# Kernel tuning notes

Measured on AMD Instinct MI355X. Metric: run time of the kernel, lower is better.

Reference implementation:

```python
import jax, jax.numpy as jnp
import numpy as np
from jax.scipy.special import gammaln

REG = 1e-6
NHLOG2PI = -0.5 * float(np.log(2.0 * np.pi))


def _log_besseli(s, kappa):
    # Uniform asymptotic expansion (leading order) of log I_s(kappa):
    # I_s(s*x) ~ exp(s*eta) / (sqrt(2*pi*s) * (1+x^2)^(1/4))
    x = kappa / s
    sq = jnp.sqrt(1.0 + x * x)
    eta = sq + jnp.log(x) - jnp.log1p(sq)
    return s * eta - 0.5 * jnp.log(2.0 * jnp.pi * s) - 0.5 * jnp.log(sq)


def _log_C_vmf(d, kappa):
    # log C_d(kappa) = d*(-0.5 log 2pi) + s*log(kappa) - log I_s(kappa), s = d/2 - 1
    s = 0.5 * d - 1.0
    return d * NHLOG2PI + s * jnp.log(kappa) - _log_besseli(s, kappa)


def _log_surface_area(dim):
    # HypersphericalUniform.__log_surface_area
    h = (dim + 1.0) / 2.0
    return np.log(2.0) + h * np.log(np.pi) - float(jax.scipy.special.gammaln(jnp.asarray(h, jnp.float32)))


def _vmf_layer(x, w_mu, w_logk, b_mu, b_logk, in_f, out_f):
    # eval mode: weight = mu (unit-normalized flat vector), reshape(in,out).T
    mu_w = w_mu / jnp.linalg.norm(w_mu)
    mu_b = b_mu / jnp.linalg.norm(b_mu)
    W = mu_w.reshape(in_f, out_f).T  # [out, in]
    y = x @ W.T + mu_b
    kw = jnp.exp(w_logk) + REG
    kb = jnp.exp(b_logk) + REG
    d_w = float(out_f * in_f)
    d_b = float(out_f)
    # log q(w) = kappa * <mu, w> + log C_d(kappa); here w = mu so <mu,w> = 1 (computed faithfully)
    lvp = (kw * jnp.dot(mu_w, mu_w) + _log_C_vmf(d_w, kw)
           + kb * jnp.dot(mu_b, mu_b) + _log_C_vmf(d_b, kb))
    # NOTE: source bug preserved -- bias prior also uses dim = out*in
    lp = -_log_surface_area(d_w) - _log_surface_area(d_w)
    return y, lvp, lp


def _gaussian_last_layer(x, w_mu, w_rho, b_mu, b_rho):
    # eval mode: weight = mu, bias = mu
    y = x @ w_mu.T + b_mu
    sw = jnp.log1p(jnp.exp(w_rho))
    sb = jnp.log1p(jnp.exp(b_rho))
    # log q at mu: (-log sqrt(2pi) - log sigma - 0).sum()
    lvp = jnp.sum(NHLOG2PI - jnp.log(sw)) + jnp.sum(NHLOG2PI - jnp.log(sb))
    # prior: PI=1, sigma1=1 -> standard normal logpdf summed
    lp = jnp.sum(NHLOG2PI - 0.5 * w_mu ** 2) + jnp.sum(NHLOG2PI - 0.5 * b_mu ** 2)
    return y, lvp, lp


def setup_inputs() -> dict:
    key = jax.random.key(0)
    ks = jax.random.split(key, 13)
    B, IN, H, OUT = 1024, 4096, 4096, 5
    return {
        "x": jax.random.normal(ks[0], (B, IN), jnp.float32),
        "w1_mu": jax.random.normal(ks[1], (H * IN,), jnp.float32),
        "w1_logkappa": jnp.float32(2.0),
        "b1_mu": jax.random.normal(ks[2], (H,), jnp.float32),
        "b1_logkappa": jnp.float32(2.0),
        "w2_mu": jax.random.normal(ks[3], (H * H,), jnp.float32),
        "w2_logkappa": jnp.float32(2.0),
        "b2_mu": jax.random.normal(ks[4], (H,), jnp.float32),
        "b2_logkappa": jnp.float32(2.0),
        "w3_mu": jax.random.uniform(ks[5], (OUT, H), jnp.float32, -0.2, 0.2),
        "w3_rho": jax.random.uniform(ks[6], (OUT, H), jnp.float32, -5.0, -4.0),
        "b3_mu": jax.random.uniform(ks[7], (OUT,), jnp.float32, -0.2, 0.2),
        "b3_rho": jax.random.uniform(ks[8], (OUT,), jnp.float32, -5.0, -4.0),
    }


def reference(x, w1_mu, w1_logkappa, b1_mu, b1_logkappa,
              w2_mu, w2_logkappa, b2_mu, b2_logkappa,
              w3_mu, w3_rho, b3_mu, b3_rho):
    IN, H, OUT = 4096, 4096, 5
    h1, lvp1, lp1 = _vmf_layer(x, w1_mu, w1_logkappa, b1_mu, b1_logkappa, IN, H)
    h1 = jax.nn.relu(h1)
    h2, lvp2, lp2 = _vmf_layer(h1, w2_mu, w2_logkappa, b2_mu, b2_logkappa, H, H)
    h2 = jax.nn.relu(h2)
    y, lvp3, lp3 = _gaussian_last_layer(h2, w3_mu, w3_rho, b3_mu, b3_rho)
    out = jax.nn.log_softmax(y, axis=-1)
    log_var_post = lvp1 + lvp2 + lvp3
    log_prior = lp1 + lp2 + lp3
    return out, log_var_post, jnp.asarray(log_prior, out.dtype)
```

## Files before the change

kernel.cpp:

```cpp
#include <hip/hip_runtime.h>
#include <cstdint>


#define NH (-0.9189385332046727)
#define DPI 3.141592653589793238462643383279502884

typedef short s16x8 __attribute__((ext_vector_type(8)));
typedef float f32x4 __attribute__((ext_vector_type(4)));

static __device__ __forceinline__ ushort f2bf(float f) {
  uint32_t u = __float_as_uint(f);
  u += 0x7fffu + ((u >> 16) & 1u);
  return (ushort)(u >> 16);
}
static __device__ __forceinline__ float bf2f(ushort h) {
  return __uint_as_float(((uint32_t)h) << 16);
}

static __device__ __forceinline__ void gload16(const void* g, void* l) {
  __builtin_amdgcn_global_load_lds(
      (__attribute__((address_space(1))) void*)g,
      (__attribute__((address_space(3))) void*)l,
      16, 0, 0);
}

__global__ void reduce_k(const float* __restrict__ x, int n,
                         double* __restrict__ part, int mode) {
  double a = 0.0;
  const int tid = blockIdx.x * blockDim.x + threadIdx.x;
  const int stride = gridDim.x * blockDim.x;
  const int n4 = n >> 2;
  for (int i = tid; i < n4; i += stride) {
    float4 v = reinterpret_cast<const float4*>(x)[i];
    if (mode == 0) {
      a += (double)v.x * v.x + (double)v.y * v.y +
           (double)v.z * v.z + (double)v.w * v.w;
    } else {
      a += log(log1p(exp((double)v.x)));
      a += log(log1p(exp((double)v.y)));
      a += log(log1p(exp((double)v.z)));
      a += log(log1p(exp((double)v.w)));
    }
  }
  for (int i = (n4 << 2) + tid; i < n; i += stride) {
    float v = x[i];
    a += (mode == 0) ? (double)v * v : log(log1p(exp((double)v)));
  }
  for (int o = 32; o > 0; o >>= 1) a += __shfl_down(a, o);
  __shared__ double red[4];
  if ((threadIdx.x & 63) == 0) red[threadIdx.x >> 6] = a;
  __syncthreads();
  if (threadIdx.x == 0) part[blockIdx.x] = red[0] + red[1] + red[2] + red[3];
}

__global__ void norms_k(const double* __restrict__ pw, int nw,
                        const double* __restrict__ pb, int nb,
                        float* __restrict__ out2) {
  __shared__ double red[4];
  const int t = threadIdx.x;
  double s[2];
  const double* p[2] = {pw, pb};
  const int   cn[2] = {nw, nb};
  for (int q = 0; q < 2; q++) {
    double v = 0.0;
    for (int i = t; i < cn[q]; i += 256) v += p[q][i];
    for (int o = 32; o > 0; o >>= 1) v += __shfl_down(v, o);
    if ((t & 63) == 0) red[t >> 6] = v;
    __syncthreads();
    s[q] = red[0] + red[1] + red[2] + red[3];
    __syncthreads();
  }
  if (t == 0) {
    out2[0] = (float)(1.0 / sqrt(s[0]));
    out2[1] = (float)(1.0 / sqrt(s[1]));
  }
}

static __device__ double logC_vmf(double d, double kappa) {
  double s  = 0.5 * d - 1.0;
  double x  = kappa / s;
  double sq = sqrt(1.0 + x * x);
  double eta = sq + log(x) - log1p(sq);
  double lb  = s * eta - 0.5 * log(2.0 * DPI * s) - 0.5 * log(sq);
  return d * NH + s * log(kappa) - lb;
}

__global__ void finalize_k(const double* __restrict__ P,
                           const float* lkw1, const float* lkb1,
                           const float* lkw2, const float* lkb2,
                           float* __restrict__ out_sc) {
  __shared__ double S[8];
  __shared__ double red[4];
  const int offs[8] = {0, 16384, 8192, 16392, 16400, 16408, 16409, 16417};
  const int cnts[8] = {8192, 8, 8192, 8, 8, 1, 8, 1};
  const int t = threadIdx.x;
  for (int ai = 0; ai < 8; ai++) {
    double v = 0.0;
    for (int i = t; i < cnts[ai]; i += 256) v += P[offs[ai] + i];
    for (int o = 32; o > 0; o >>= 1) v += __shfl_down(v, o);
    if ((t & 63) == 0) red[t >> 6] = v;
    __syncthreads();
    if (t == 0) S[ai] = red[0] + red[1] + red[2] + red[3];
    __syncthreads();
  }
  if (t == 0) {
    double Sw3 = S[4], Sb3 = S[5], R6 = S[6], R7 = S[7];
    const double dw = 16777216.0, db = 4096.0;
    double kw1 = exp((double)lkw1[0]) + 1e-6;
    double kb1 = exp((double)lkb1[0]) + 1e-6;
    double kw2 = exp((double)lkw2[0]) + 1e-6;
    double kb2 = exp((double)lkb2[0]) + 1e-6;
    double lvp = kw1 + logC_vmf(dw, kw1) + kb1 + logC_vmf(db, kb1)
               + kw2 + logC_vmf(dw, kw2) + kb2 + logC_vmf(db, kb2)
               + 20485.0 * NH - R6 - R7;
    double h64 = (dw + 1.0) * 0.5;
    double hf  = (double)(float)h64;
    double lsa = log(2.0) + h64 * log(DPI) - lgamma(hf);
    double lp  = -4.0 * lsa + 20485.0 * NH - 0.5 * (Sw3 + Sb3);
    out_sc[0] = (float)lvp;
    out_sc[1] = (float)lp;
  }
}

__global__ void split_plain_k(const float* __restrict__ in,
                              ushort* __restrict__ hi, ushort* __restrict__ lo,
                              int n4) {
  int i = blockIdx.x * blockDim.x + threadIdx.x;
  if (i >= n4) return;
  float4 v = reinterpret_cast<const float4*>(in)[i];
  ushort4 h, l;
  h.x = f2bf(v.x); l.x = f2bf(v.x - bf2f(h.x));
  h.y = f2bf(v.y); l.y = f2bf(v.y - bf2f(h.y));
  h.z = f2bf(v.z); l.z = f2bf(v.z - bf2f(h.z));
  h.w = f2bf(v.w); l.w = f2bf(v.w - bf2f(h.w));
  reinterpret_cast<ushort4*>(hi)[i] = h;
  reinterpret_cast<ushort4*>(lo)[i] = l;
}

__global__ void split_transpose_k(const float* __restrict__ in,
                                  ushort* __restrict__ hi,
                                  ushort* __restrict__ lo,
                                  double* __restrict__ part) {
  __shared__ float tile[64][33];
  __shared__ double red[4];
  const int tx = threadIdx.x, ty = threadIdx.y;
  const int n0 = blockIdx.x * 32, k0 = blockIdx.y * 64;
  double a = 0.0;
#pragma unroll
  for (int r = 0; r < 8; r++) {
    float v = in[(size_t)(k0 + ty + r * 8) * 4096 + n0 + tx];
    tile[ty + r * 8][tx] = v;
    a += (double)v * v;
  }
  __syncthreads();
#pragma unroll
  for (int r = 0; r < 4; r++) {
    const int nn = ty + r * 8;
    float v0 = tile[2 * tx][nn];
    float v1 = tile[2 * tx + 1][nn];
    ushort2 h, l;
    h.x = f2bf(v0); l.x = f2bf(v0 - bf2f(h.x));
    h.y = f2bf(v1); l.y = f2bf(v1 - bf2f(h.y));
    size_t o = ((size_t)(n0 + nn) * 4096 + k0 + 2 * tx) >> 1;
    reinterpret_cast<ushort2*>(hi)[o] = h;
    reinterpret_cast<ushort2*>(lo)[o] = l;
  }
  const int tid = ty * 32 + tx;
  for (int o = 32; o > 0; o >>= 1) a += __shfl_down(a, o);
  if ((tid & 63) == 0) red[tid >> 6] = a;
  __syncthreads();
  if (tid == 0)
    part[blockIdx.y * gridDim.x + blockIdx.x] = red[0] + red[1] + red[2] + red[3];
}

__global__ __launch_bounds__(256) void gemm_split_k(
    const ushort* __restrict__ Ahi, const ushort* __restrict__ Alo,
    const ushort* __restrict__ Bhi, const ushort* __restrict__ Blo,
    const float* __restrict__ bias, const float* __restrict__ scales,
    ushort* __restrict__ Ohi, ushort* __restrict__ Olo,
    float* __restrict__ Of,
    int M, int N, int K, int mode) {
  __shared__ ushort As[2][2][64 * 32];
  __shared__ ushort Bs[2][2][128 * 32];
  const int t = threadIdx.x;
  const int lane = t & 63, wid = t >> 6;
  const int wm = wid >> 1, wn = wid & 1;
  const int bm = blockIdx.y, bn = blockIdx.x;
  const int lr = lane & 15, lk = (lane >> 4) * 8;

  f32x4 acc[2][4];
#pragma unroll
  for (int i = 0; i < 2; i++)
#pragma unroll
    for (int j = 0; j < 4; j++) acc[i][j] = (f32x4){0.f, 0.f, 0.f, 0.f};

  const size_t arow = (size_t)(bm * 64) * K;
  const size_t brow = (size_t)(bn * 128) * K;
  const int ar = t >> 2, ac = (t & 3) * 8;

  auto STAGE = [&](int buf, int k0) {
    const size_t ga = arow + (size_t)ar * K + k0 + ac;
    gload16(Ahi + ga, &As[buf][0][t * 8]);
    gload16(Alo + ga, &As[buf][1][t * 8]);
#pragma unroll
    for (int q = 0; q < 2; q++) {
      const int L = q * 256 + t;
      const size_t gb = brow + (size_t)(L >> 2) * K + k0 + (L & 3) * 8;
      gload16(Bhi + gb, &Bs[buf][0][L * 8]);
      gload16(Blo + gb, &Bs[buf][1][L * 8]);
    }
  };

  auto COMPUTE = [&](int buf) {
    s16x8 ah[2], al[2], bh[4], bl[4];
#pragma unroll
    for (int i = 0; i < 2; i++) {
      const int ra = (wm * 32 + i * 16 + lr) * 32 + lk;
      ah[i] = *(const s16x8*)&As[buf][0][ra];
      al[i] = *(const s16x8*)&As[buf][1][ra];
    }
#pragma unroll
    for (int j = 0; j < 4; j++) {
      const int rb = (wn * 64 + j * 16 + lr) * 32 + lk;
      bh[j] = *(const s16x8*)&Bs[buf][0][rb];
      bl[j] = *(const s16x8*)&Bs[buf][1][rb];
    }
#pragma unroll
    for (int i = 0; i < 2; i++)
#pragma unroll
      for (int j = 0; j < 4; j++) {
        acc[i][j] = __builtin_amdgcn_mfma_f32_16x16x32_bf16(ah[i], bh[j], acc[i][j], 0, 0, 0);
        acc[i][j] = __builtin_amdgcn_mfma_f32_16x16x32_bf16(ah[i], bl[j], acc[i][j], 0, 0, 0);
        acc[i][j] = __builtin_amdgcn_mfma_f32_16x16x32_bf16(al[i], bh[j], acc[i][j], 0, 0, 0);
      }
  };

  STAGE(0, 0);
  __syncthreads();
  int cur = 0;
  for (int k0 = 32; k0 < K; k0 += 32) {
    STAGE(cur ^ 1, k0);
    COMPUTE(cur);
    __syncthreads();
    cur ^= 1;
  }
  COMPUTE(cur);

  const float wsc = scales[0], bsc = scales[1];
  const int rb0 = bm * 64 + wm * 32 + (lane >> 4) * 4;
  const int cb0 = bn * 128 + wn * 64 + lr;
#pragma unroll
  for (int j = 0; j < 4; j++) {
    const int col = cb0 + j * 16;
    const float bv = bias[col] * bsc;
#pragma unroll
    for (int i = 0; i < 2; i++) {
#pragma unroll
      for (int r = 0; r < 4; r++) {
        const int row = rb0 + i * 16 + r;
        float v = fmaxf(fmaf(acc[i][j][r], wsc, bv), 0.0f);
        const size_t o = (size_t)row * N + col;
        if (mode == 0) {
          ushort h = f2bf(v);
          Ohi[o] = h;
          Olo[o] = f2bf(v - bf2f(h));
        } else {
          Of[o] = v;
        }
      }
    }
  }
}

__global__ void layer3_k(const float* __restrict__ h2,
                         const float* __restrict__ w3,
                         const float* __restrict__ b3,
                         float* __restrict__ out) {
  const int row = blockIdx.x;
  const int t = threadIdx.x;
  const float* hr = h2 + (size_t)row * 4096;
  float a[5] = {0.f, 0.f, 0.f, 0.f, 0.f};
  for (int k = t; k < 4096; k += 256) {
    const float h = hr[k];
#pragma unroll
    for (int o = 0; o < 5; o++) a[o] += h * w3[o * 4096 + k];
  }
#pragma unroll
  for (int o = 0; o < 5; o++)
    for (int s = 32; s > 0; s >>= 1) a[o] += __shfl_down(a[o], s);
  __shared__ float red[4][5];
  if ((t & 63) == 0) {
#pragma unroll
    for (int o = 0; o < 5; o++) red[t >> 6][o] = a[o];
  }
  __syncthreads();
  if (t == 0) {
    float y[5];
#pragma unroll
    for (int o = 0; o < 5; o++)
      y[o] = red[0][o] + red[1][o] + red[2][o] + red[3][o] + b3[o];
    float m = y[0];
    for (int o = 1; o < 5; o++) m = fmaxf(m, y[o]);
    float ssum = 0.f;
    for (int o = 0; o < 5; o++) ssum += expf(y[o] - m);
    const float ls = m + logf(ssum);
    for (int o = 0; o < 5; o++) out[row * 5 + o] = y[o] - ls;
  }
}

extern "C" void kernel_launch(void* const* d_in, const int* in_sizes, int n_in,
                              void* d_out, int out_size, void* d_ws, size_t ws_size,
                              hipStream_t stream) {
  const float* x     = (const float*)d_in[0];
  const float* w1mu  = (const float*)d_in[1];
  const float* lkw1  = (const float*)d_in[2];
  const float* b1mu  = (const float*)d_in[3];
  const float* lkb1  = (const float*)d_in[4];
  const float* w2mu  = (const float*)d_in[5];
  const float* lkw2  = (const float*)d_in[6];
  const float* b2mu  = (const float*)d_in[7];
  const float* lkb2  = (const float*)d_in[8];
  const float* w3mu  = (const float*)d_in[9];
  const float* w3rho = (const float*)d_in[10];
  const float* b3mu  = (const float*)d_in[11];
  const float* b3rho = (const float*)d_in[12];
  float* outp = (float*)d_out;

  char* w = (char*)d_ws;
  double* P    = (double*)w;
  double* Pw1  = P;
  double* Pw2  = P + 8192;
  double* Pb1  = P + 16384;
  double* Pb2  = P + 16392;
  double* Pw3  = P + 16400;
  double* Pb3  = P + 16408;
  double* Pr3  = P + 16409;
  double* Pbr3 = P + 16417;
  float* params = (float*)(w + 140 * 1024);
  ushort* xhi  = (ushort*)(w + 256 * 1024);
  ushort* xlo  = xhi  + (size_t)1024 * 4096;
  ushort* h1hi = xlo  + (size_t)1024 * 4096;
  ushort* h1lo = h1hi + (size_t)1024 * 4096;
  ushort* wthi = (ushort*)(h1lo + (size_t)1024 * 4096);
  ushort* wtlo = wthi + (size_t)4096 * 4096;
  float*  h2   = (float*)xhi;

  split_plain_k<<<4096, 256, 0, stream>>>(x, xhi, xlo, 1048576);
  split_transpose_k<<<dim3(128, 64), dim3(32, 8), 0, stream>>>(w1mu, wthi, wtlo, Pw1);
  reduce_k<<<8, 256, 0, stream>>>(b1mu, 4096, Pb1, 0);
  reduce_k<<<8, 256, 0, stream>>>(w3mu, 20480, Pw3, 0);
  reduce_k<<<1, 256, 0, stream>>>(b3mu, 5, Pb3, 0);
  reduce_k<<<8, 256, 0, stream>>>(w3rho, 20480, Pr3, 1);
  reduce_k<<<1, 256, 0, stream>>>(b3rho, 5, Pbr3, 1);
  norms_k<<<1, 256, 0, stream>>>(Pw1, 8192, Pb1, 8, params + 0);
  gemm_split_k<<<dim3(32, 16), 256, 0, stream>>>(xhi, xlo, wthi, wtlo,
                                                 b1mu, params + 0,
                                                 h1hi, h1lo, nullptr,
                                                 1024, 4096, 4096, 0);
  split_transpose_k<<<dim3(128, 64), dim3(32, 8), 0, stream>>>(w2mu, wthi, wtlo, Pw2);
  reduce_k<<<8, 256, 0, stream>>>(b2mu, 4096, Pb2, 0);
  norms_k<<<1, 256, 0, stream>>>(Pw2, 8192, Pb2, 8, params + 2);
  gemm_split_k<<<dim3(32, 16), 256, 0, stream>>>(h1hi, h1lo, wthi, wtlo,
                                                 b2mu, params + 2,
                                                 nullptr, nullptr, h2,
                                                 1024, 4096, 4096, 1);
  finalize_k<<<1, 256, 0, stream>>>(P, lkw1, lkb1, lkw2, lkb2, outp + 5120);
  layer3_k<<<1024, 256, 0, stream>>>(h2, w3mu, b3mu, outp);
}
```

Measured before the change: 568.4 us.

## Split GEMM K dimension in two with combine kernel and merge small reductions

Adds a split-K mode to the bf16x3 GEMM, launching twice as many blocks that each cover half of K. The blocks write fp32 partials, and a separate combine kernel applies scale, bias, ReLU and the hi/lo split. The goal is better CU occupancy for a 512-block grid. LDS double buffering is removed in favour of a single-buffer loop with two barriers. Small reductions are merged into one launch. The change adds partial-buffer traffic and loses the load/compute overlap, and it is gated on workspace size.

```diff
diff --git a/kernel.cpp b/kernel.cpp
--- a/kernel.cpp
+++ b/kernel.cpp
@@ -24,25 +24,24 @@
       16, 0, 0);
 }
 
-__global__ void reduce_k(const float* __restrict__ x, int n,
-                         double* __restrict__ part, int mode) {
+__global__ void small_reduce_k(const float* __restrict__ b1,
+                               const float* __restrict__ b2,
+                               const float* __restrict__ w3,
+                               const float* __restrict__ b3,
+                               const float* __restrict__ r3,
+                               const float* __restrict__ br3,
+                               double* __restrict__ P) {
+  const int bid = blockIdx.x;
+  const float* x; int n, lb, nb, mode; double* out;
+  if (bid < 8)        { x = b1;  n = 4096;  lb = bid;      nb = 8; mode = 0; out = P + 16384; }
+  else if (bid < 16)  { x = b2;  n = 4096;  lb = bid - 8;  nb = 8; mode = 0; out = P + 16392; }
+  else if (bid < 24)  { x = w3;  n = 20480; lb = bid - 16; nb = 8; mode = 0; out = P + 16400; }
+  else if (bid == 24) { x = b3;  n = 5;     lb = 0;        nb = 1; mode = 0; out = P + 16408; }
+  else if (bid < 33)  { x = r3;  n = 20480; lb = bid - 25; nb = 8; mode = 1; out = P + 16409; }
+  else                { x = br3; n = 5;     lb = 0;        nb = 1; mode = 1; out = P + 16417; }
   double a = 0.0;
-  const int tid = blockIdx.x * blockDim.x + threadIdx.x;
-  const int stride = gridDim.x * blockDim.x;
-  const int n4 = n >> 2;
-  for (int i = tid; i < n4; i += stride) {
-    float4 v = reinterpret_cast<const float4*>(x)[i];
-    if (mode == 0) {
-      a += (double)v.x * v.x + (double)v.y * v.y +
-           (double)v.z * v.z + (double)v.w * v.w;
-    } else {
-      a += log(log1p(exp((double)v.x)));
-      a += log(log1p(exp((double)v.y)));
-      a += log(log1p(exp((double)v.z)));
-      a += log(log1p(exp((double)v.w)));
-    }
-  }
-  for (int i = (n4 << 2) + tid; i < n; i += stride) {
+  const int tid = lb * 256 + threadIdx.x, stride = nb * 256;
+  for (int i = tid; i < n; i += stride) {
     float v = x[i];
     a += (mode == 0) ? (double)v * v : log(log1p(exp((double)v)));
   }
@@ -50,7 +49,7 @@
   __shared__ double red[4];
   if ((threadIdx.x & 63) == 0) red[threadIdx.x >> 6] = a;
   __syncthreads();
-  if (threadIdx.x == 0) part[blockIdx.x] = red[0] + red[1] + red[2] + red[3];
+  if (threadIdx.x == 0) out[lb] = red[0] + red[1] + red[2] + red[3];
 }
 
 __global__ void norms_k(const double* __restrict__ pw, int nw,
@@ -179,9 +178,9 @@
     const float* __restrict__ bias, const float* __restrict__ scales,
     ushort* __restrict__ Ohi, ushort* __restrict__ Olo,
     float* __restrict__ Of,
-    int M, int N, int K, int mode) {
-  __shared__ ushort As[2][2][64 * 32];
-  __shared__ ushort Bs[2][2][128 * 32];
+    int M, int N, int K, int ksize, int mode) {
+  __shared__ ushort As[2][64 * 32];
+  __shared__ ushort Bs[2][128 * 32];
   const int t = threadIdx.x;
   const int lane = t & 63, wid = t >> 6;
   const int wm = wid >> 1, wn = wid & 1;
@@ -197,33 +196,35 @@
   const size_t arow = (size_t)(bm * 64) * K;
   const size_t brow = (size_t)(bn * 128) * K;
   const int ar = t >> 2, ac = (t & 3) * 8;
-
-  auto STAGE = [&](int buf, int k0) {
-    const size_t ga = arow + (size_t)ar * K + k0 + ac;
-    gload16(Ahi + ga, &As[buf][0][t * 8]);
-    gload16(Alo + ga, &As[buf][1][t * 8]);
+  const int kbeg = blockIdx.z * ksize;
+  const int kend = kbeg + ksize;
+
+  for (int k0 = kbeg; k0 < kend; k0 += 32) {
+    {
+      const size_t ga = arow + (size_t)ar * K + k0 + ac;
+      gload16(Ahi + ga, &As[0][t * 8]);
+      gload16(Alo + ga, &As[1][t * 8]);
+    }
 #pragma unroll
     for (int q = 0; q < 2; q++) {
       const int L = q * 256 + t;
       const size_t gb = brow + (size_t)(L >> 2) * K + k0 + (L & 3) * 8;
-      gload16(Bhi + gb, &Bs[buf][0][L * 8]);
-      gload16(Blo + gb, &Bs[buf][1][L * 8]);
-    }
-  };
-
-  auto COMPUTE = [&](int buf) {
+      gload16(Bhi + gb, &Bs[0][L * 8]);
+      gload16(Blo + gb, &Bs[1][L * 8]);
+    }
+    __syncthreads();
     s16x8 ah[2], al[2], bh[4], bl[4];
 #pragma unroll
     for (int i = 0; i < 2; i++) {
       const int ra = (wm * 32 + i * 16 + lr) * 32 + lk;
-      ah[i] = *(const s16x8*)&As[buf][0][ra];
-      al[i] = *(const s16x8*)&As[buf][1][ra];
+      ah[i] = *(const s16x8*)&As[0][ra];
+      al[i] = *(const s16x8*)&As[1][ra];
     }
 #pragma unroll
     for (int j = 0; j < 4; j++) {
       const int rb = (wn * 64 + j * 16 + lr) * 32 + lk;
-      bh[j] = *(const s16x8*)&Bs[buf][0][rb];
-      bl[j] = *(const s16x8*)&Bs[buf][1][rb];
+      bh[j] = *(const s16x8*)&Bs[0][rb];
+      bl[j] = *(const s16x8*)&Bs[1][rb];
     }
 #pragma unroll
     for (int i = 0; i < 2; i++)
@@ -233,22 +234,25 @@
         acc[i][j] = __builtin_amdgcn_mfma_f32_16x16x32_bf16(ah[i], bl[j], acc[i][j], 0, 0, 0);
         acc[i][j] = __builtin_amdgcn_mfma_f32_16x16x32_bf16(al[i], bh[j], acc[i][j], 0, 0, 0);
       }
-  };
-
-  STAGE(0, 0);
-  __syncthreads();
-  int cur = 0;
-  for (int k0 = 32; k0 < K; k0 += 32) {
-    STAGE(cur ^ 1, k0);
-    COMPUTE(cur);
-    __syncthreads();
-    cur ^= 1;
-  }
-  COMPUTE(cur);
-
-  const float wsc = scales[0], bsc = scales[1];
+    __syncthreads();
+  }
+
   const int rb0 = bm * 64 + wm * 32 + (lane >> 4) * 4;
   const int cb0 = bn * 128 + wn * 64 + lr;
+  if (mode == 2) {
+    float* Op = Of + (size_t)blockIdx.z * ((size_t)M * N);
+#pragma unroll
+    for (int j = 0; j < 4; j++) {
+      const int col = cb0 + j * 16;
+#pragma unroll
+      for (int i = 0; i < 2; i++)
+#pragma unroll
+        for (int r = 0; r < 4; r++)
+          Op[(size_t)(rb0 + i * 16 + r) * N + col] = acc[i][j][r];
+    }
+    return;
+  }
+  const float wsc = scales[0], bsc = scales[1];
 #pragma unroll
   for (int j = 0; j < 4; j++) {
     const int col = cb0 + j * 16;
@@ -269,6 +273,34 @@
         }
       }
     }
+  }
+}
+
+__global__ void combine_k(const float* __restrict__ p,
+                          const float* __restrict__ bias,
+                          const float* __restrict__ sc,
+                          ushort* __restrict__ Ohi, ushort* __restrict__ Olo,
+                          float* __restrict__ Of, int mode) {
+  const int i = blockIdx.x * blockDim.x + threadIdx.x;
+  const float wsc = sc[0], bsc = sc[1];
+  float4 a = reinterpret_cast<const float4*>(p)[i];
+  float4 b = reinterpret_cast<const float4*>(p + 4194304)[i];
+  float4 bv = *reinterpret_cast<const float4*>(bias + ((i * 4) & 4095));
+  float4 v;
+  v.x = fmaxf(fmaf(a.x + b.x, wsc, bv.x * bsc), 0.f);
+  v.y = fmaxf(fmaf(a.y + b.y, wsc, bv.y * bsc), 0.f);
+  v.z = fmaxf(fmaf(a.z + b.z, wsc, bv.z * bsc), 0.f);
+  v.w = fmaxf(fmaf(a.w + b.w, wsc, bv.w * bsc), 0.f);
+  if (mode == 0) {
+    ushort4 h, l;
+    h.x = f2bf(v.x); l.x = f2bf(v.x - bf2f(h.x));
+    h.y = f2bf(v.y); l.y = f2bf(v.y - bf2f(h.y));
+    h.z = f2bf(v.z); l.z = f2bf(v.z - bf2f(h.z));
+    h.w = f2bf(v.w); l.w = f2bf(v.w - bf2f(h.w));
+    reinterpret_cast<ushort4*>(Ohi)[i] = h;
+    reinterpret_cast<ushort4*>(Olo)[i] = l;
+  } else {
+    reinterpret_cast<float4*>(Of)[i] = v;
   }
 }
 
@@ -330,12 +362,6 @@
   double* P    = (double*)w;
   double* Pw1  = P;
   double* Pw2  = P + 8192;
-  double* Pb1  = P + 16384;
-  double* Pb2  = P + 16392;
-  double* Pw3  = P + 16400;
-  double* Pb3  = P + 16408;
-  double* Pr3  = P + 16409;
-  double* Pbr3 = P + 16417;
   float* params = (float*)(w + 140 * 1024);
   ushort* xhi  = (ushort*)(w + 256 * 1024);
   ushort* xlo  = xhi  + (size_t)1024 * 4096;
@@ -343,27 +369,39 @@
   ushort* h1lo = h1hi + (size_t)1024 * 4096;
   ushort* wthi = (ushort*)(h1lo + (size_t)1024 * 4096);
   ushort* wtlo = wthi + (size_t)4096 * 4096;
+  float*  part = (float*)(wtlo + (size_t)4096 * 4096);
   float*  h2   = (float*)xhi;
+
+  const bool splitk = ws_size >= (size_t)134479872;
 
   split_plain_k<<<4096, 256, 0, stream>>>(x, xhi, xlo, 1048576);
   split_transpose_k<<<dim3(128, 64), dim3(32, 8), 0, stream>>>(w1mu, wthi, wtlo, Pw1);
-  reduce_k<<<8, 256, 0, stream>>>(b1mu, 4096, Pb1, 0);
-  reduce_k<<<8, 256, 0, stream>>>(w3mu, 20480, Pw3, 0);
-  reduce_k<<<1, 256, 0, stream>>>(b3mu, 5, Pb3, 0);
-  reduce_k<<<8, 256, 0, stream>>>(w3rho, 20480, Pr3, 1);
-  reduce_k<<<1, 256, 0, stream>>>(b3rho, 5, Pbr3, 1);
-  norms_k<<<1, 256, 0, stream>>>(Pw1, 8192, Pb1, 8, params + 0);
-  gemm_split_k<<<dim3(32, 16), 256, 0, stream>>>(xhi, xlo, wthi, wtlo,
-                                                 b1mu, params + 0,
-                                                 h1hi, h1lo, nullptr,
-                                                 1024, 4096, 4096, 0);
+  small_reduce_k<<<34, 256, 0, stream>>>(b1mu, b2mu, w3mu, b3mu, w3rho, b3rho, P);
+  norms_k<<<1, 256, 0, stream>>>(Pw1, 8192, P + 16384, 8, params + 0);
+  if (splitk) {
+    gemm_split_k<<<dim3(32, 16, 2), 256, 0, stream>>>(
+        xhi, xlo, wthi, wtlo, nullptr, nullptr, nullptr, nullptr, part,
+        1024, 4096, 4096, 2048, 2);
+    combine_k<<<4096, 256, 0, stream>>>(part, b1mu, params + 0,
+                                        h1hi, h1lo, nullptr, 0);
+  } else {
+    gemm_split_k<<<dim3(32, 16, 1), 256, 0, stream>>>(
+        xhi, xlo, wthi, wtlo, b1mu, params + 0, h1hi, h1lo, nullptr,
+        1024, 4096, 4096, 4096, 0);
+  }
   split_transpose_k<<<dim3(128, 64), dim3(32, 8), 0, stream>>>(w2mu, wthi, wtlo, Pw2);
-  reduce_k<<<8, 256, 0, stream>>>(b2mu, 4096, Pb2, 0);
-  norms_k<<<1, 256, 0, stream>>>(Pw2, 8192, Pb2, 8, params + 2);
-  gemm_split_k<<<dim3(32, 16), 256, 0, stream>>>(h1hi, h1lo, wthi, wtlo,
-                                                 b2mu, params + 2,
-                                                 nullptr, nullptr, h2,
-                                                 1024, 4096, 4096, 1);
+  norms_k<<<1, 256, 0, stream>>>(Pw2, 8192, P + 16392, 8, params + 2);
+  if (splitk) {
+    gemm_split_k<<<dim3(32, 16, 2), 256, 0, stream>>>(
+        h1hi, h1lo, wthi, wtlo, nullptr, nullptr, nullptr, nullptr, part,
+        1024, 4096, 4096, 2048, 2);
+    combine_k<<<4096, 256, 0, stream>>>(part, b2mu, params + 2,
+                                        nullptr, nullptr, h2, 1);
+  } else {
+    gemm_split_k<<<dim3(32, 16, 1), 256, 0, stream>>>(
+        h1hi, h1lo, wthi, wtlo, b2mu, params + 2, nullptr, nullptr, h2,
+        1024, 4096, 4096, 4096, 1);
+  }
   finalize_k<<<1, 256, 0, stream>>>(P, lkw1, lkb1, lkw2, lkb2, outp + 5120);
   layer3_k<<<1024, 256, 0, stream>>>(h2, w3mu, b3mu, outp);
 }
```

Result: faster. 527.2 us (-7.2%).
